# Optimization experiments

Hardware: AMD Instinct MI355X
Metric: run time of the kernel (lower is better)

## Reference

```python
import jax, jax.numpy as jnp
import numpy as np

EMB, NH, NG, T_MAX = 2048, 16, 4, 2048
HD = EMB // NH          # 128
HPG = NH // NG          # 4
B, T = 2, 2048


def _rope_tables(t):
    inv_freq = 1.0 / (10000.0 ** (jnp.arange(0, HD, 2, dtype=jnp.float32) / HD))
    freqs = jnp.outer(jnp.arange(t, dtype=jnp.float32), inv_freq)  # [t, HD//2]
    return jnp.cos(freqs), jnp.sin(freqs)


def _apply_rope(x, cos, sin):
    # x: [..., t, HD], interleaved pairs (0::2 real, 1::2 imag)
    x1 = x[..., 0::2]
    x2 = x[..., 1::2]
    r1 = x1 * cos - x2 * sin
    r2 = x1 * sin + x2 * cos
    return jnp.stack([r1, r2], axis=-1).reshape(x.shape)


def setup_inputs() -> dict:
    key = jax.random.key(0)
    ks = jax.random.split(key, 5)
    s = 0.02
    return {
        "x": jax.random.normal(ks[0], (B, T, EMB), dtype=jnp.float32),
        "Wq": jax.random.normal(ks[1], (EMB, EMB), dtype=jnp.float32) * s,
        "Wk": jax.random.normal(ks[2], (NG * HD, EMB), dtype=jnp.float32) * s,
        "Wv": jax.random.normal(ks[3], (NG * HD, EMB), dtype=jnp.float32) * s,
        "Wo": jax.random.normal(ks[4], (EMB, EMB), dtype=jnp.float32) * s,
    }


def reference(x, Wq, Wk, Wv, Wo):
    b, t, _ = x.shape
    cos, sin = _rope_tables(t)  # [t, HD//2] each; broadcast over batch/heads

    # projections (torch Linear: x @ W.T)
    q = (x @ Wq.T).reshape(b, t, NH, HD).transpose(0, 2, 1, 3)  # [b, NH, t, HD]
    k = (x @ Wk.T).reshape(b, t, NG, HD).transpose(0, 2, 1, 3)  # [b, NG, t, HD]
    v = (x @ Wv.T).reshape(b, t, NG, HD).transpose(0, 2, 1, 3)  # [b, NG, t, HD]

    q = _apply_rope(q, cos, sin)
    k = _apply_rope(k, cos, sin)

    # grouped attention without materializing expanded K/V
    qg = q.reshape(b, NG, HPG, t, HD)                       # [b, g, h, t, d]
    scale = 1.0 / jnp.sqrt(jnp.asarray(HD, dtype=x.dtype))
    scores = jnp.einsum('bghtd,bgsd->bghts', qg, k) * scale  # [b, g, h, t, s]

    causal = jnp.tril(jnp.ones((t, t), dtype=bool))
    scores = jnp.where(causal, scores, jnp.finfo(scores.dtype).min)
    attn = jax.nn.softmax(scores, axis=-1)

    out = jnp.einsum('bghts,bgsd->bghtd', attn, v)           # [b, g, h, t, d]
    out = out.reshape(b, NH, t, HD).transpose(0, 2, 1, 3).reshape(b, t, EMB)
    return out @ Wo.T
```

## Files before the change

### kernel.cpp

```cpp
#include <hip/hip_runtime.h>
#include <stdint.h>
#include <math.h>

#define EMB 2048
#define NHq 16
#define NGk 4
#define HD 128
#define Bb 2
#define Tt 2048
#define MROWS (Bb*Tt)
#define QKVN 3072
#define NQT 32

typedef __bf16 bf16x8 __attribute__((ext_vector_type(8)));
typedef float f32x4 __attribute__((ext_vector_type(4)));
typedef unsigned short u16;

__device__ __forceinline__ u16 f2bf(float f) {
    unsigned int u = __float_as_uint(f);
    u += 0x7fff + ((u >> 16) & 1);
    return (u16)(u >> 16);
}

#define GLOAD_LDS16(g, l) \
    __builtin_amdgcn_global_load_lds((const __attribute__((address_space(1))) void*)(g), \
                                     (__attribute__((address_space(3))) void*)(l), 16, 0, 0)

__global__ void cast_bf16_kernel(const float* __restrict__ src, u16* __restrict__ dst, int n4) {
    int i = blockIdx.x * blockDim.x + threadIdx.x;
    if (i < n4) {
        float4 v = reinterpret_cast<const float4*>(src)[i];
        ushort4 o;
        o.x = f2bf(v.x); o.y = f2bf(v.y); o.z = f2bf(v.z); o.w = f2bf(v.w);
        reinterpret_cast<ushort4*>(dst)[i] = o;
    }
}

__global__ void rope_tables_kernel(float* __restrict__ ctab, float* __restrict__ stab) {
    int t = blockIdx.x, i = threadIdx.x;
    float inv = powf(10000.f, -2.f * (float)i / (float)HD);
    float ang = (float)t * inv;
    ctab[t * 64 + i] = cosf(ang);
    stab[t * 64 + i] = sinf(ang);
}

__global__ void rope_kernel(const float* __restrict__ lin, const float* __restrict__ ctab,
                            const float* __restrict__ stab, u16* __restrict__ out,
                            int coloff, int nh, float scale) {
    int i = threadIdx.x;
    int tt = blockIdx.x * 4 + threadIdx.y;
    int h = blockIdx.y, b = blockIdx.z;
    const float2 xv = *reinterpret_cast<const float2*>(
        &lin[((size_t)(b * Tt + tt)) * QKVN + coloff + h * HD + 2 * i]);
    float c = ctab[tt * 64 + i], s = stab[tt * 64 + i];
    ushort2 o;
    o.x = f2bf((xv.x * c - xv.y * s) * scale);
    o.y = f2bf((xv.x * s + xv.y * c) * scale);
    *reinterpret_cast<ushort2*>(&out[(((size_t)(b * nh + h)) * Tt + tt) * HD + 2 * i]) = o;
}

__global__ void vtrans_kernel(const float* __restrict__ lin, u16* __restrict__ vt) {
    int tx = threadIdx.x, dy = threadIdx.y;
    int tt = blockIdx.x * 64 + tx;
    int g = blockIdx.y, b = blockIdx.z;
    const float* src = &lin[((size_t)(b * Tt + tt)) * QKVN + EMB + NGk * HD + g * HD];
    u16* dst = &vt[(((size_t)(b * NGk + g)) * HD) * Tt + tt];
    #pragma unroll
    for (int k = 0; k < 16; ++k) {
        int d = dy + k * 8;
        dst[(size_t)d * Tt] = f2bf(src[d]);
    }
}

__global__ __launch_bounds__(256) void gemm_bt(const u16* __restrict__ A, const u16* __restrict__ W,
                                               float* __restrict__ C, int M, int N, int K) {
    __shared__ u16 Atile[128 * 32];
    __shared__ u16 Btile[128 * 32];
    const int brow = blockIdx.x * 128;
    const int bcol = blockIdx.y * 128;
    const int t = threadIdx.x;
    const int w = t >> 6, l = t & 63;
    const int lr = l & 15, lq = l >> 4;
    const int wr = (w >> 1) * 64, wc = (w & 1) * 64;
    f32x4 acc[4][4] = {};
    const int nkt = K >> 5;
    for (int kt = 0; kt < nkt; ++kt) {
        const int k0 = kt * 32;
        #pragma unroll
        for (int i = 0; i < 2; ++i) {
            int f = i * 256 + t;
            int row = f >> 2, cb = (f & 3) * 8;
            GLOAD_LDS16(A + (size_t)(brow + row) * K + k0 + cb, &Atile[(i * 256 + w * 64) * 8]);
            GLOAD_LDS16(W + (size_t)(bcol + row) * K + k0 + cb, &Btile[(i * 256 + w * 64) * 8]);
        }
        __syncthreads();
        bf16x8 a[4], b[4];
        #pragma unroll
        for (int m = 0; m < 4; ++m)
            a[m] = *reinterpret_cast<const bf16x8*>(&Atile[(wr + m * 16 + lr) * 32 + lq * 8]);
        #pragma unroll
        for (int n = 0; n < 4; ++n)
            b[n] = *reinterpret_cast<const bf16x8*>(&Btile[(wc + n * 16 + lr) * 32 + lq * 8]);
        #pragma unroll
        for (int m = 0; m < 4; ++m)
            #pragma unroll
            for (int n = 0; n < 4; ++n)
                acc[m][n] = __builtin_amdgcn_mfma_f32_16x16x32_bf16(a[m], b[n], acc[m][n], 0, 0, 0);
        __syncthreads();
    }
    #pragma unroll
    for (int m = 0; m < 4; ++m)
        #pragma unroll
        for (int n = 0; n < 4; ++n)
            #pragma unroll
            for (int r = 0; r < 4; ++r)
                C[(size_t)(brow + wr + m * 16 + lq * 4 + r) * N + bcol + wc + n * 16 + lr] = acc[m][n][r];
}

__global__ __launch_bounds__(256) void flash_attn(const u16* __restrict__ Q, const u16* __restrict__ K,
                                                  const u16* __restrict__ Vt, u16* __restrict__ Out) {
    __shared__ u16 Klds[2][64 * 128];
    __shared__ u16 Vlds[2][128 * 64];
    __shared__ u16 Plds[4][16 * 64];
    const int ilo = blockIdx.x;
    const int ihi = NQT - 1 - ilo;
    const int h = blockIdx.y;
    const int b = blockIdx.z;
    const int g = h >> 2;
    const int t = threadIdx.x;
    const int w = t >> 6, l = t & 63;
    const int lr = l & 15, lq = l >> 4;

    const size_t qhead = ((size_t)(b * NHq + h)) * Tt;
    const size_t qblo = (qhead + ilo * 64 + w * 16) * HD;
    const size_t qbhi = (qhead + ihi * 64 + w * 16) * HD;
    bf16x8 qfl[4], qfh[4];
    #pragma unroll
    for (int d = 0; d < 4; ++d) {
        qfl[d] = *reinterpret_cast<const bf16x8*>(&Q[qblo + (size_t)lr * HD + d * 32 + lq * 8]);
        qfh[d] = *reinterpret_cast<const bf16x8*>(&Q[qbhi + (size_t)lr * HD + d * 32 + lq * 8]);
    }
    bf16x8 ones;
    #pragma unroll
    for (int j = 0; j < 8; ++j) ones[j] = (__bf16)1.0f;

    f32x4 ol[8] = {}, oh[8] = {};
    f32x4 lsum_l = {}, lsum_h = {};

    const int qlo0 = ilo * 64 + w * 16 + lq * 4;
    const int qhi0 = ihi * 64 + w * 16 + lq * 4;
    const size_t kbase  = ((size_t)(b * NGk + g)) * Tt * HD;
    const size_t vtbase = ((size_t)(b * NGk + g)) * HD * Tt;
    const int nkt = NQT - ilo;

    int kofs[4], vofs[4];
    #pragma unroll
    for (int j = 0; j < 4; ++j) {
        int blk = j * 4 + w;
        int krow = blk * 4 + (l >> 4);
        int kcb = (l & 15) ^ (krow & 7);
        kofs[j] = krow * HD + kcb * 8;
        int vd = blk * 8 + (l >> 3);
        int vseg = (l & 7) ^ (vd & 7);
        vofs[j] = vd * Tt + vseg * 8;
    }

    #pragma unroll
    for (int j = 0; j < 4; ++j) {
        int blk = j * 4 + w;
        GLOAD_LDS16(K + kbase + kofs[j], &Klds[0][blk * 512]);
        GLOAD_LDS16(Vt + vtbase + vofs[j], &Vlds[0][blk * 512]);
    }
    int cur = 0;

    for (int kt = 0; kt < nkt; ++kt) {
        const int kp0 = kt * 64;
        __syncthreads();
        if (kt + 1 < nkt) {
            const int kp1 = kp0 + 64;
            #pragma unroll
            for (int j = 0; j < 4; ++j) {
                int blk = j * 4 + w;
                GLOAD_LDS16(K + kbase + (size_t)kp1 * HD + kofs[j], &Klds[cur ^ 1][blk * 512]);
                GLOAD_LDS16(Vt + vtbase + kp1 + vofs[j], &Vlds[cur ^ 1][blk * 512]);
            }
        }
        const u16* Kb = Klds[cur];
        const u16* Vb = Vlds[cur];

        const bool lo_act = (kt <= ilo);
        f32x4 sl[4] = {}, sh[4] = {};
        __builtin_amdgcn_s_setprio(1);
        #pragma unroll
        for (int ct = 0; ct < 4; ++ct) {
            #pragma unroll
            for (int d = 0; d < 4; ++d) {
                int row = ct * 16 + lr;
                int bo = row * 256 + ((d * 64 + lq * 16) ^ ((row & 7) << 4));
                bf16x8 kf = *reinterpret_cast<const bf16x8*>((const char*)Kb + bo);
                if (lo_act) sl[ct] = __builtin_amdgcn_mfma_f32_16x16x32_bf16(qfl[d], kf, sl[ct], 0, 0, 0);
                sh[ct] = __builtin_amdgcn_mfma_f32_16x16x32_bf16(qfh[d], kf, sh[ct], 0, 0, 0);
            }
        }
        __builtin_amdgcn_s_setprio(0);

        {
            const bool diag = (kt == nkt - 1);
            #pragma unroll
            for (int ct = 0; ct < 4; ++ct)
                #pragma unroll
                for (int r = 0; r < 4; ++r) {
                    float v = sh[ct][r];
                    if (diag && (kp0 + ct * 16 + lr > qhi0 + r)) v = -1e30f;
                    int row = lq * 4 + r;
                    int bo = row * 128 + (((ct * 16 + lr) * 2) ^ ((row & 7) << 4));
                    *reinterpret_cast<u16*>((char*)Plds[w] + bo) = f2bf(exp2f(v));
                }
        }
        bf16x8 pfh0, pfh1;
        {
            int bo0 = lr * 128 + ((lq * 16) ^ ((lr & 7) << 4));
            int bo1 = lr * 128 + ((64 + lq * 16) ^ ((lr & 7) << 4));
            pfh0 = *reinterpret_cast<const bf16x8*>((const char*)Plds[w] + bo0);
            pfh1 = *reinterpret_cast<const bf16x8*>((const char*)Plds[w] + bo1);
        }
        bf16x8 pfl0, pfl1;
        if (lo_act) {
            const bool diag = (kt == ilo);
            #pragma unroll
            for (int ct = 0; ct < 4; ++ct)
                #pragma unroll
                for (int r = 0; r < 4; ++r) {
                    float v = sl[ct][r];
                    if (diag && (kp0 + ct * 16 + lr > qlo0 + r)) v = -1e30f;
                    int row = lq * 4 + r;
                    int bo = row * 128 + (((ct * 16 + lr) * 2) ^ ((row & 7) << 4));
                    *reinterpret_cast<u16*>((char*)Plds[w] + bo) = f2bf(exp2f(v));
                }
            int bo0 = lr * 128 + ((lq * 16) ^ ((lr & 7) << 4));
            int bo1 = lr * 128 + ((64 + lq * 16) ^ ((lr & 7) << 4));
            pfl0 = *reinterpret_cast<const bf16x8*>((const char*)Plds[w] + bo0);
            pfl1 = *reinterpret_cast<const bf16x8*>((const char*)Plds[w] + bo1);
        }

        __builtin_amdgcn_s_setprio(1);
        #pragma unroll
        for (int n = 0; n < 8; ++n) {
            int dcol = n * 16 + lr;
            int bv0 = dcol * 128 + ((lq * 16) ^ ((dcol & 7) << 4));
            int bv1 = dcol * 128 + ((64 + lq * 16) ^ ((dcol & 7) << 4));
            bf16x8 vf0 = *reinterpret_cast<const bf16x8*>((const char*)Vb + bv0);
            bf16x8 vf1 = *reinterpret_cast<const bf16x8*>((const char*)Vb + bv1);
            oh[n] = __builtin_amdgcn_mfma_f32_16x16x32_bf16(pfh0, vf0, oh[n], 0, 0, 0);
            oh[n] = __builtin_amdgcn_mfma_f32_16x16x32_bf16(pfh1, vf1, oh[n], 0, 0, 0);
            if (lo_act) {
                ol[n] = __builtin_amdgcn_mfma_f32_16x16x32_bf16(pfl0, vf0, ol[n], 0, 0, 0);
                ol[n] = __builtin_amdgcn_mfma_f32_16x16x32_bf16(pfl1, vf1, ol[n], 0, 0, 0);
            }
        }
        lsum_h = __builtin_amdgcn_mfma_f32_16x16x32_bf16(pfh0, ones, lsum_h, 0, 0, 0);
        lsum_h = __builtin_amdgcn_mfma_f32_16x16x32_bf16(pfh1, ones, lsum_h, 0, 0, 0);
        if (lo_act) {
            lsum_l = __builtin_amdgcn_mfma_f32_16x16x32_bf16(pfl0, ones, lsum_l, 0, 0, 0);
            lsum_l = __builtin_amdgcn_mfma_f32_16x16x32_bf16(pfl1, ones, lsum_l, 0, 0, 0);
        }
        __builtin_amdgcn_s_setprio(0);
        cur ^= 1;
    }

    float invl[4], invh[4];
    #pragma unroll
    for (int r = 0; r < 4; ++r) { invl[r] = 1.f / lsum_l[r]; invh[r] = 1.f / lsum_h[r]; }
    const size_t obase = ((size_t)b * Tt) * EMB + (size_t)h * HD;
    #pragma unroll
    for (int n = 0; n < 8; ++n)
        #pragma unroll
        for (int r = 0; r < 4; ++r) {
            int rl = ilo * 64 + w * 16 + lq * 4 + r;
            int rh = ihi * 64 + w * 16 + lq * 4 + r;
            Out[obase + (size_t)rl * EMB + n * 16 + lr] = f2bf(ol[n][r] * invl[r]);
            Out[obase + (size_t)rh * EMB + n * 16 + lr] = f2bf(oh[n][r] * invh[r]);
        }
}

extern "C" void kernel_launch(void* const* d_in, const int* in_sizes, int n_in,
                              void* d_out, int out_size, void* d_ws, size_t ws_size,
                              hipStream_t stream) {
    (void)in_sizes; (void)n_in; (void)out_size; (void)ws_size;
    const float* x  = (const float*)d_in[0];
    const float* Wq = (const float*)d_in[1];
    const float* Wk = (const float*)d_in[2];
    const float* Wv = (const float*)d_in[3];
    const float* Wo = (const float*)d_in[4];
    float* out = (float*)d_out;

    char* ws = (char*)d_ws;
    size_t off = 0;
    auto alloc = [&](size_t bytes) { char* p = ws + off; off += (bytes + 255) & ~(size_t)255; return p; };

    u16* w_bf    = (u16*)alloc((size_t)(QKVN * EMB + EMB * EMB) * 2);
    u16* x_bf    = (u16*)alloc((size_t)MROWS * EMB * 2);
    float* qkv_lin = (float*)alloc((size_t)MROWS * QKVN * 4);
    u16* Qb      = (u16*)alloc((size_t)Bb * NHq * Tt * HD * 2);
    u16* Kb      = (u16*)alloc((size_t)Bb * NGk * Tt * HD * 2);
    u16* Vtb     = (u16*)alloc((size_t)Bb * NGk * HD * Tt * 2);
    float* ctab  = (float*)alloc((size_t)Tt * 64 * 4);
    float* stab  = (float*)alloc((size_t)Tt * 64 * 4);
    u16* attnout = (u16*)qkv_lin;

    u16* wq_bf = w_bf;
    u16* wk_bf = w_bf + (size_t)EMB * EMB;
    u16* wv_bf = wk_bf + (size_t)NGk * HD * EMB;
    u16* wo_bf = wv_bf + (size_t)NGk * HD * EMB;

    cast_bf16_kernel<<<(MROWS * EMB / 4 + 255) / 256, 256, 0, stream>>>(x, x_bf, MROWS * EMB / 4);
    cast_bf16_kernel<<<(EMB * EMB / 4 + 255) / 256, 256, 0, stream>>>(Wq, wq_bf, EMB * EMB / 4);
    cast_bf16_kernel<<<(NGk * HD * EMB / 4 + 255) / 256, 256, 0, stream>>>(Wk, wk_bf, NGk * HD * EMB / 4);
    cast_bf16_kernel<<<(NGk * HD * EMB / 4 + 255) / 256, 256, 0, stream>>>(Wv, wv_bf, NGk * HD * EMB / 4);
    cast_bf16_kernel<<<(EMB * EMB / 4 + 255) / 256, 256, 0, stream>>>(Wo, wo_bf, EMB * EMB / 4);
    rope_tables_kernel<<<Tt, 64, 0, stream>>>(ctab, stab);

    gemm_bt<<<dim3(MROWS / 128, QKVN / 128), 256, 0, stream>>>(x_bf, w_bf, qkv_lin, MROWS, QKVN, EMB);

    const float qscale = 1.44269504088896f / sqrtf((float)HD);
    rope_kernel<<<dim3(Tt / 4, NHq, Bb), dim3(64, 4), 0, stream>>>(qkv_lin, ctab, stab, Qb, 0, NHq, qscale);
    rope_kernel<<<dim3(Tt / 4, NGk, Bb), dim3(64, 4), 0, stream>>>(qkv_lin, ctab, stab, Kb, EMB, NGk, 1.0f);
    vtrans_kernel<<<dim3(Tt / 64, NGk, Bb), dim3(64, 8), 0, stream>>>(qkv_lin, Vtb);

    flash_attn<<<dim3(NQT / 2, NHq, Bb), 256, 0, stream>>>(Qb, Kb, Vtb, attnout);

    gemm_bt<<<dim3(MROWS / 128, EMB / 128), 256, 0, stream>>>(attnout, wo_bf, out, MROWS, EMB, EMB);
}
```

Baseline: 262.4 us.

## Permute V key order so P tiles pack into vectorized bf16 LDS stores

The transposed V buffer now stores key positions in a permuted order within each 64-key block. The P-tile writes in attention can then group four column tiles per lane into one 8-byte LDS store, using the hardware packed bf16 convert. This replaces sixteen scalar 2-byte stores and software rounding per half-tile. The permutation has to match exactly between the V layout and the P columns, otherwise the P·V product pairs the wrong keys.

```diff
diff --git a/kernel.cpp b/kernel.cpp
--- a/kernel.cpp
+++ b/kernel.cpp
@@ -20,6 +20,12 @@
     unsigned int u = __float_as_uint(f);
     u += 0x7fff + ((u >> 16) & 1);
     return (u16)(u >> 16);
+}
+
+__device__ __forceinline__ unsigned int cvt_pk_bf16(float lo, float hi) {
+    unsigned int r;
+    asm("v_cvt_pk_bf16_f32 %0, %1, %2" : "=v"(r) : "v"(lo), "v"(hi));
+    return r;
 }
 
 #define GLOAD_LDS16(g, l) \
@@ -63,8 +69,9 @@
     int tx = threadIdx.x, dy = threadIdx.y;
     int tt = blockIdx.x * 64 + tx;
     int g = blockIdx.y, b = blockIdx.z;
+    int ttp = (tt & ~63) | (((tt & 15) << 2) | ((tt >> 4) & 3));
     const float* src = &lin[((size_t)(b * Tt + tt)) * QKVN + EMB + NGk * HD + g * HD];
-    u16* dst = &vt[(((size_t)(b * NGk + g)) * HD) * Tt + tt];
+    u16* dst = &vt[(((size_t)(b * NGk + g)) * HD) * Tt + ttp];
     #pragma unroll
     for (int k = 0; k < 16; ++k) {
         int d = dy + k * 8;
@@ -206,16 +213,24 @@
 
         {
             const bool diag = (kt == nkt - 1);
+            float e[4][4];
             #pragma unroll
             for (int ct = 0; ct < 4; ++ct)
                 #pragma unroll
                 for (int r = 0; r < 4; ++r) {
                     float v = sh[ct][r];
                     if (diag && (kp0 + ct * 16 + lr > qhi0 + r)) v = -1e30f;
-                    int row = lq * 4 + r;
-                    int bo = row * 128 + (((ct * 16 + lr) * 2) ^ ((row & 7) << 4));
-                    *reinterpret_cast<u16*>((char*)Plds[w] + bo) = f2bf(exp2f(v));
+                    e[ct][r] = exp2f(v);
                 }
+            #pragma unroll
+            for (int r = 0; r < 4; ++r) {
+                int row = lq * 4 + r;
+                uint2 pk;
+                pk.x = cvt_pk_bf16(e[0][r], e[1][r]);
+                pk.y = cvt_pk_bf16(e[2][r], e[3][r]);
+                int bo = row * 128 + ((lr * 8) ^ ((row & 7) << 4));
+                *reinterpret_cast<uint2*>((char*)Plds[w] + bo) = pk;
+            }
         }
         bf16x8 pfh0, pfh1;
         {
@@ -227,16 +242,24 @@
         bf16x8 pfl0, pfl1;
         if (lo_act) {
             const bool diag = (kt == ilo);
+            float e[4][4];
             #pragma unroll
             for (int ct = 0; ct < 4; ++ct)
                 #pragma unroll
                 for (int r = 0; r < 4; ++r) {
                     float v = sl[ct][r];
                     if (diag && (kp0 + ct * 16 + lr > qlo0 + r)) v = -1e30f;
-                    int row = lq * 4 + r;
-                    int bo = row * 128 + (((ct * 16 + lr) * 2) ^ ((row & 7) << 4));
-                    *reinterpret_cast<u16*>((char*)Plds[w] + bo) = f2bf(exp2f(v));
+                    e[ct][r] = exp2f(v);
                 }
+            #pragma unroll
+            for (int r = 0; r < 4; ++r) {
+                int row = lq * 4 + r;
+                uint2 pk;
+                pk.x = cvt_pk_bf16(e[0][r], e[1][r]);
+                pk.y = cvt_pk_bf16(e[2][r], e[3][r]);
+                int bo = row * 128 + ((lr * 8) ^ ((row & 7) << 4));
+                *reinterpret_cast<uint2*>((char*)Plds[w] + bo) = pk;
+            }
             int bo0 = lr * 128 + ((lq * 16) ^ ((lr & 7) << 4));
             int bo1 = lr * 128 + ((64 + lq * 16) ^ ((lr & 7) << 4));
             pfl0 = *reinterpret_cast<const bf16x8*>((const char*)Plds[w] + bo0);
```

Result: no change. 257.7 us (-1.8%).
